# Optimization experiments

Measured on AMD Instinct MI355X. Metric: run time of the kernel, lower is better.

The kernel has to match this reference:

```python
import jax, jax.numpy as jnp
import numpy as np
import math

D_MODEL = 512
N_HEADS = 8
D_FF = 2048
TOP_FACTOR = 5
LN_EPS = 1e-5


def _layernorm(x, g, b):
    m = jnp.mean(x, axis=-1, keepdims=True)
    v = jnp.mean((x - m) ** 2, axis=-1, keepdims=True)
    return (x - m) / jnp.sqrt(v + LN_EPS) * g + b


def _prob_sparse_attn(q_in, k_in, v_in, wq, bq, wk, bk, wv, bv, wo, bo):
    # weights stored (in, out): y = x @ w + b  (equivalent to torch Linear)
    B, Lq, dm = q_in.shape
    Lk = k_in.shape[1]
    H, D = N_HEADS, dm // N_HEADS
    q = (q_in @ wq + bq).reshape(B, Lq, H, D).transpose(0, 2, 1, 3)  # (B,H,Lq,D)
    k = (k_in @ wk + bk).reshape(B, Lk, H, D).transpose(0, 2, 1, 3)
    v = (v_in @ wv + bv).reshape(B, Lk, H, D).transpose(0, 2, 1, 3)

    qn = q / jnp.linalg.norm(q, axis=-1, keepdims=True)
    kn = k / jnp.linalg.norm(k, axis=-1, keepdims=True)
    # full cosine-similarity matrix, reduced to a row mean (as in the original)
    scores_all = jnp.einsum('bhqd,bhkd->bhqk', qn, kn)
    mean_scores = scores_all.mean(axis=-1)  # (B,H,Lq)

    u = max(1, Lq // TOP_FACTOR)
    _, top_idx = jax.lax.top_k(mean_scores, u)  # (B,H,u)

    q_sel = jnp.take_along_axis(q, top_idx[..., None], axis=2)  # (B,H,u,D)
    scores = jnp.einsum('bhud,bhkd->bhuk', q_sel, k) / math.sqrt(D)
    attn = jax.nn.softmax(scores, axis=-1)
    ctx_sel = jnp.einsum('bhuk,bhkd->bhud', attn, v)  # (B,H,u,D)

    b_ix = jnp.arange(B)[:, None, None]
    h_ix = jnp.arange(H)[None, :, None]
    context = jnp.zeros((B, H, Lq, D), dtype=q.dtype).at[b_ix, h_ix, top_idx].set(ctx_sel)
    out = context.transpose(0, 2, 1, 3).reshape(B, Lq, dm)
    return out @ wo + bo


def _decoder_layer(x, enc_out, p):
    xn = _layernorm(x, p['ln1_g'], p['ln1_b'])
    x = x + _prob_sparse_attn(xn, xn, xn, p['sa_wq'], p['sa_bq'], p['sa_wk'], p['sa_bk'],
                              p['sa_wv'], p['sa_bv'], p['sa_wo'], p['sa_bo'])
    xn = _layernorm(x, p['ln2_g'], p['ln2_b'])
    x = x + _prob_sparse_attn(xn, enc_out, enc_out, p['ca_wq'], p['ca_bq'], p['ca_wk'], p['ca_bk'],
                              p['ca_wv'], p['ca_bv'], p['ca_wo'], p['ca_bo'])
    xn = _layernorm(x, p['ln3_g'], p['ln3_b'])
    h = jax.nn.relu(xn @ p['ff_w1'] + p['ff_b1'])
    return x + (h @ p['ff_w2'] + p['ff_b2'])


def setup_inputs() -> dict:
    key = jax.random.key(0)
    ks = iter(jax.random.split(key, 32))
    B, L = 2, 2048
    dm, dff = D_MODEL, D_FF
    s = 1.0 / math.sqrt(dm)
    inp = {
        'x': jax.random.normal(next(ks), (B, L, dm), jnp.float32),
        'enc_out': jax.random.normal(next(ks), (B, L, dm), jnp.float32),
    }
    for pre in ('sa', 'ca'):
        for nm in ('wq', 'wk', 'wv', 'wo'):
            inp[f'{pre}_{nm}'] = jax.random.normal(next(ks), (dm, dm), jnp.float32) * s
            inp[f'{pre}_{nm[1:] and "b" + nm[1:]}'] = jnp.zeros((dm,), jnp.float32)
    inp['ff_w1'] = jax.random.normal(next(ks), (dm, dff), jnp.float32) * s
    inp['ff_b1'] = jnp.zeros((dff,), jnp.float32)
    inp['ff_w2'] = jax.random.normal(next(ks), (dff, dm), jnp.float32) / math.sqrt(dff)
    inp['ff_b2'] = jnp.zeros((dm,), jnp.float32)
    for i in (1, 2, 3):
        inp[f'ln{i}_g'] = jnp.ones((dm,), jnp.float32)
        inp[f'ln{i}_b'] = jnp.zeros((dm,), jnp.float32)
    return inp


def reference(x, enc_out,
              sa_wq, sa_bq, sa_wk, sa_bk, sa_wv, sa_bv, sa_wo, sa_bo,
              ca_wq, ca_bq, ca_wk, ca_bk, ca_wv, ca_bv, ca_wo, ca_bo,
              ff_w1, ff_b1, ff_w2, ff_b2,
              ln1_g, ln1_b, ln2_g, ln2_b, ln3_g, ln3_b):
    p = dict(sa_wq=sa_wq, sa_bq=sa_bq, sa_wk=sa_wk, sa_bk=sa_bk, sa_wv=sa_wv, sa_bv=sa_bv,
             sa_wo=sa_wo, sa_bo=sa_bo, ca_wq=ca_wq, ca_bq=ca_bq, ca_wk=ca_wk, ca_bk=ca_bk,
             ca_wv=ca_wv, ca_bv=ca_bv, ca_wo=ca_wo, ca_bo=ca_bo,
             ff_w1=ff_w1, ff_b1=ff_b1, ff_w2=ff_w2, ff_b2=ff_b2,
             ln1_g=ln1_g, ln1_b=ln1_b, ln2_g=ln2_g, ln2_b=ln2_b, ln3_g=ln3_g, ln3_b=ln3_b)
    return _decoder_layer(x, enc_out, p)
```

## Files before the change

kernel.cpp:

```cpp
#include <hip/hip_runtime.h>

#define BB 2
#define LL 2048
#define DM 512
#define NH 8
#define DH 64
#define DFF 2048
#define UU 409
#define ROWS (BB*LL)
#define X_ELEMS 2097152
#define NCHUNK 8

typedef unsigned short u16;
typedef __attribute__((ext_vector_type(8))) short short8;
typedef __attribute__((ext_vector_type(4))) float floatx4;

#define G_TOTAL 38200000
__device__ float g_buf[G_TOTAL];
__device__ int   g_isbf16;

#define A_Q     10495488
#define A_K     12592640
#define A_V     14689792
#define A_MKN   25175552
#define A_MS    25176576
#define A_RANK  25209344
#define A_PARTK 25242112
#define A_LIST  25274880
#define A_PO    25281536
#define A_PML   29475840
#define A_CTXF  16786944
#define XN_H    16796672
#define XN_L    18893824
#define CTX_H   33573888
#define CTX_L   35671040
#define ENC_H   37768192
#define ENC_L   39865344
#define AH_H    41962496
#define KH16    59213824
#define KL16    61310976
#define VTH16   63408128
#define VTL16   65505280
#define WT_SAQKV 67864576
#define WT_SAO   69437440
#define WT_CAQ   69961728
#define WT_CAKV  70486016
#define WT_CAO   71534592
#define WT_W1    72058880
#define WT_W2    74156032

__constant__ int c_end[28] = {
    2097152, 4194304, 4456448, 4456960, 4719104, 4719616, 4981760, 4982272,
    5244416, 5244928, 5507072, 5507584, 5769728, 5770240, 6032384, 6032896,
    6295040, 6295552, 7344128, 7346176, 8394752, 8395264, 8395776, 8396288,
    8396800, 8397312, 8397824, 8398336
};
__constant__ int sm_idx[16] = {3,5,7,9,11,13,15,17,19,21,22,23,24,25,26,27};
__constant__ int sm_cum[16] = {64,128,192,256,320,384,448,512,768,832,896,960,1024,1088,1152,1216};
#define XG 262144
#define EG 262144
#define SG 1216

__device__ __forceinline__ float bf2f(u16 x) {
    union { unsigned int u; float f; } c; c.u = ((unsigned int)x) << 16; return c.f;
}
__device__ __forceinline__ u16 f2bf(float f) {
    union { float f; unsigned int u; } c; c.f = f;
    unsigned int u = c.u;
    return (u16)((u + 0x7FFFu + ((u >> 16) & 1u)) >> 16);
}

struct P28 { const void* p[28]; };
struct I3 { int v[3]; };

__constant__ int tj[10][6] = {
    {2,  WT_SAQKV, 0,    512,  786432, 8},
    {4,  WT_SAQKV, 512,  512,  786432, 8},
    {6,  WT_SAQKV, 1024, 512,  786432, 8},
    {8,  WT_SAO,   0,    512,  262144, 8},
    {10, WT_CAQ,   0,    512,  262144, 8},
    {12, WT_CAKV,  0,    512,  524288, 8},
    {14, WT_CAKV,  512,  512,  524288, 8},
    {16, WT_CAO,   0,    512,  262144, 8},
    {18, WT_W1,    0,    512, 1048576, 32},
    {20, WT_W2,    0,   2048, 1048576, 8},
};
__constant__ int tcum[10] = {64, 128, 192, 256, 320, 384, 448, 512, 768, 1024};
__global__ void prep_all(P28 ps) {
    const int f = (((const u16*)ps.p[22])[0] == 0x3F80u) ? 1 : 0;
    if (blockIdx.x == 0 && threadIdx.x == 0) g_isbf16 = f;
    u16* gb16 = (u16*)g_buf;
    if (blockIdx.x < 1024) {
        int bid = blockIdx.x;
        int j = 0;
        while (bid >= tcum[j]) j++;
        int t = bid - (j ? tcum[j - 1] : 0);
        int widx = tj[j][0], wt = tj[j][1], col0 = tj[j][2];
        int K = tj[j][3], lo = tj[j][4], txn = tj[j][5];
        int Nsrc = txn * 64;
        int n0 = (t % txn) * 64, k0 = (t / txn) * 64;
        __shared__ float tb[64][65];
        int c = threadIdx.x & 63, r0 = threadIdx.x >> 6;
        const void* W = ps.p[widx];
        u16* WTh = gb16 + wt;
        for (int i = 0; i < 16; i++) {
            int r = r0 + 4 * i;
            size_t src = (size_t)(k0 + r) * Nsrc + n0 + c;
            tb[r][c] = f ? bf2f(((const u16*)W)[src]) : ((const float*)W)[src];
        }
        __syncthreads();
        for (int i = 0; i < 16; i++) {
            int r = r0 + 4 * i;
            float v = tb[c][r];
            u16 hi = f2bf(v);
            size_t o = (size_t)(col0 + n0 + r) * K + k0 + c;
            WTh[o] = hi;
            WTh[lo + o] = f2bf(v - bf2f(hi));
        }
        return;
    }
    int stride = 2048 * blockDim.x;
    for (int g = (blockIdx.x - 1024) * blockDim.x + threadIdx.x; g < XG + EG + SG; g += stride) {
        if (g < XG) {
            int e = g * 8;
            if (f) {
                uint4 raw = ((const uint4*)ps.p[0])[g];
                const u16* rr = (const u16*)&raw;
                float v[8] __attribute__((aligned(16)));
#pragma unroll
                for (int i = 0; i < 8; i++) v[i] = bf2f(rr[i]);
                *(float4*)(g_buf + e) = ((const float4*)v)[0];
                *(float4*)(g_buf + e + 4) = ((const float4*)v)[1];
            } else {
                *(uint4*)(g_buf + e)     = ((const uint4*)ps.p[0])[g * 2];
                *(uint4*)(g_buf + e + 4) = ((const uint4*)ps.p[0])[g * 2 + 1];
            }
        } else if (g < XG + EG) {
            int gl = g - XG;
            int e = gl * 8;
            float v[8] __attribute__((aligned(16)));
            if (f) {
                uint4 raw = ((const uint4*)ps.p[1])[gl];
                const u16* rr = (const u16*)&raw;
#pragma unroll
                for (int i = 0; i < 8; i++) v[i] = bf2f(rr[i]);
            } else {
                *(float4*)(v)     = ((const float4*)ps.p[1])[gl * 2];
                *(float4*)(v + 4) = ((const float4*)ps.p[1])[gl * 2 + 1];
            }
            u16 hh[8] __attribute__((aligned(16)));
            u16 lo[8] __attribute__((aligned(16)));
#pragma unroll
            for (int i = 0; i < 8; i++) { u16 hi = f2bf(v[i]); hh[i] = hi; lo[i] = f2bf(v[i] - bf2f(hi)); }
            *(uint4*)(&gb16[ENC_H + e]) = *(const uint4*)hh;
            *(uint4*)(&gb16[ENC_L + e]) = *(const uint4*)lo;
        } else {
            int t = g - XG - EG;
            int si = 0;
            while (t >= sm_cum[si]) si++;
            int s = sm_idx[si];
            int gl = t - (si ? sm_cum[si - 1] : 0);
            int e = gl * 8;
            float* dst = g_buf + c_end[s - 1] + e;
            if (f) {
                uint4 raw = *(const uint4*)((const u16*)ps.p[s] + e);
                const u16* rr = (const u16*)&raw;
#pragma unroll
                for (int i = 0; i < 8; i++) dst[i] = bf2f(rr[i]);
            } else {
                *(uint4*)(dst)     = *(const uint4*)((const float*)ps.p[s] + e);
                *(uint4*)(dst + 4) = *(const uint4*)((const float*)ps.p[s] + e + 4);
            }
        }
    }
}

__global__ void lnorm_k(int x_off, int g_off, int b_off, int yh_u16, int yl_u16) {
    int row = blockIdx.x;
    int tid = threadIdx.x;
    const float* x = g_buf + x_off + (size_t)row * DM;
    float a = x[tid], c = x[tid + 256];
    float s1 = a + c, s2 = a * a + c * c;
    for (int o = 32; o > 0; o >>= 1) { s1 += __shfl_xor(s1, o); s2 += __shfl_xor(s2, o); }
    __shared__ float r1[4], r2[4];
    int wave = tid >> 6, lane = tid & 63;
    if (lane == 0) { r1[wave] = s1; r2[wave] = s2; }
    __syncthreads();
    s1 = r1[0] + r1[1] + r1[2] + r1[3];
    s2 = r2[0] + r2[1] + r2[2] + r2[3];
    float mean = s1 * (1.0f / DM);
    float var  = s2 * (1.0f / DM) - mean * mean;
    float rstd = rsqrtf(var + 1e-5f);
    const float* gg = g_buf + g_off;
    const float* bb = g_buf + b_off;
    u16* yh = ((u16*)g_buf) + yh_u16 + (size_t)row * DM;
    u16* yl = ((u16*)g_buf) + yl_u16 + (size_t)row * DM;
    float v1 = (a - mean) * rstd * gg[tid]       + bb[tid];
    float v2 = (c - mean) * rstd * gg[tid + 256] + bb[tid + 256];
    u16 h1 = f2bf(v1), h2 = f2bf(v2);
    yh[tid] = h1;       yl[tid] = f2bf(v1 - bf2f(h1));
    yh[tid + 256] = h2; yl[tid + 256] = f2bf(v2 - bf2f(h2));
}

template<int WM, bool SPLIT, bool SEC, bool RELU, bool RESID, bool FINAL, bool OUTH>
__global__ void mgemm_k(I3 a_offs, I3 splt, I3 alz, int wt_u16_off, I3 boffs, int resid_off,
                        int out_off, void* __restrict__ dext, int M, int N, int K) {
    constexpr int BT_M = WM * 32;
    constexpr int A4 = BT_M * 4;
    __shared__ u16 Ash[BT_M * 40];
    __shared__ u16 Asl[SPLIT ? BT_M * 40 : 8];
    __shared__ u16 Bsh[128 * 40];
    __shared__ u16 Bsl[SPLIT ? 128 * 40 : 8];
    int sec_blk = SEC ? ((blockIdx.x * 128) >> 9) : 0;
    const u16* Ah = ((const u16*)g_buf) + a_offs.v[sec_blk];
    const u16* Al = Ah + (size_t)M * K;
    const u16* WTh = ((const u16*)g_buf) + wt_u16_off;
    const u16* WTl = WTh + (size_t)N * K;
    const int isbf = g_isbf16;
    const bool use_al = SPLIT && splt.v[sec_blk] && !(alz.v[sec_blk] && isbf);
    const bool use_bl = SPLIT && splt.v[sec_blk] && !isbf;
    int tid = threadIdx.x;
    int lane = tid & 63, wid = tid >> 6;
    int wm = wid >> 1, wn = wid & 1;
    int quad = lane >> 4, l15 = lane & 15;
    int m0 = blockIdx.y * BT_M, n0 = blockIdx.x * 128;
    floatx4 acc[WM][4];
#pragma unroll
    for (int i = 0; i < WM; i++)
#pragma unroll
        for (int j = 0; j < 4; j++) acc[i][j] = (floatx4){0.f, 0.f, 0.f, 0.f};
    for (int k0 = 0; k0 < K; k0 += 32) {
#pragma unroll
        for (int i = 0; i < (A4 + 255) / 256; i++) {
            int idx8 = tid + 256 * i;
            if (A4 % 256 == 0 || idx8 < A4) {
                int r = idx8 >> 2, c8 = (idx8 & 3) * 8;
                *(uint4*)(&Ash[r * 40 + c8]) = *(const uint4*)(Ah + (size_t)(m0 + r) * K + k0 + c8);
                if (SPLIT && use_al)
                    *(uint4*)(&Asl[r * 40 + c8]) = *(const uint4*)(Al + (size_t)(m0 + r) * K + k0 + c8);
            }
        }
#pragma unroll
        for (int i = 0; i < 2; i++) {
            int idx8 = tid + 256 * i;
            int r = idx8 >> 2, c8 = (idx8 & 3) * 8;
            *(uint4*)(&Bsh[r * 40 + c8]) = *(const uint4*)(WTh + (size_t)(n0 + r) * K + k0 + c8);
            if (SPLIT && use_bl)
                *(uint4*)(&Bsl[r * 40 + c8]) = *(const uint4*)(WTl + (size_t)(n0 + r) * K + k0 + c8);
        }
        __syncthreads();
        short8 ah[WM], bh[4], al[WM], bl[4];
#pragma unroll
        for (int i = 0; i < WM; i++) {
            int ro = (wm * WM * 16 + i * 16 + l15) * 40 + quad * 8;
            ah[i] = *(const short8*)(&Ash[ro]);
            if (SPLIT && use_al) al[i] = *(const short8*)(&Asl[ro]);
        }
#pragma unroll
        for (int j = 0; j < 4; j++) {
            int ro = (wn * 64 + j * 16 + l15) * 40 + quad * 8;
            bh[j] = *(const short8*)(&Bsh[ro]);
            if (SPLIT && use_bl) bl[j] = *(const short8*)(&Bsl[ro]);
        }
#pragma unroll
        for (int i = 0; i < WM; i++)
#pragma unroll
            for (int j = 0; j < 4; j++) {
                acc[i][j] = __builtin_amdgcn_mfma_f32_16x16x32_bf16(ah[i], bh[j], acc[i][j], 0, 0, 0);
                if constexpr (SPLIT) {
                    if (use_bl)
                        acc[i][j] = __builtin_amdgcn_mfma_f32_16x16x32_bf16(ah[i], bl[j], acc[i][j], 0, 0, 0);
                    if (use_al)
                        acc[i][j] = __builtin_amdgcn_mfma_f32_16x16x32_bf16(al[i], bh[j], acc[i][j], 0, 0, 0);
                }
            }
        __syncthreads();
    }
#pragma unroll
    for (int i = 0; i < WM; i++)
#pragma unroll
        for (int j = 0; j < 4; j++)
#pragma unroll
            for (int r = 0; r < 4; r++) {
                int row = m0 + wm * WM * 16 + i * 16 + quad * 4 + r;
                int col = n0 + wn * 64 + j * 16 + l15;
                int sec = SEC ? (col >> 9) : 0;
                int ci  = SEC ? (col & 511) : col;
                float v = acc[i][j][r] + g_buf[boffs.v[sec] + ci];
                if (RELU) v = fmaxf(v, 0.f);
                if (RESID) v += g_buf[resid_off + (size_t)row * N + col];
                if (FINAL) {
                    if (g_isbf16) ((u16*)dext)[(size_t)row * N + col] = f2bf(v);
                    else          ((float*)dext)[(size_t)row * N + col] = v;
                } else if (OUTH) {
                    ((u16*)g_buf)[out_off + (size_t)row * N + col] = f2bf(v);
                } else if (SEC) {
                    g_buf[out_off + ((size_t)sec * ROWS + row) * 512 + ci] = v;
                } else {
                    g_buf[out_off + (size_t)row * N + col] = v;
                }
            }
}

__global__ void meankn_p1(int k_off, int part_off) {
    int bh = blockIdx.x >> 5, chunk = blockIdx.x & 31;
    int b = bh >> 3, h = bh & 7;
    int wave = threadIdx.x >> 6, lane = threadIdx.x & 63;
    const float* base = g_buf + k_off + (size_t)b * LL * DM + (size_t)h * DH + lane;
    float acc = 0.f;
    for (int t = 0; t < 16; t++) {
        int j = chunk * 64 + wave * 16 + t;
        float kv = base[(size_t)j * DM];
        float s = kv * kv;
        for (int o = 32; o > 0; o >>= 1) s += __shfl_xor(s, o);
        acc += kv / sqrtf(fmaxf(s, 1e-30f));
    }
    __shared__ float red[4][64];
    red[wave][lane] = acc;
    __syncthreads();
    if (threadIdx.x < 64)
        g_buf[part_off + (size_t)blockIdx.x * 64 + threadIdx.x] =
            red[0][threadIdx.x] + red[1][threadIdx.x] + red[2][threadIdx.x] + red[3][threadIdx.x];
}

__global__ void mscore_k(int q_off, int part_off, int ms_off) {
    int bh = blockIdx.y, b = bh >> 3, h = bh & 7;
    int tid = threadIdx.x;
    __shared__ float mk[64];
    if (tid < 64) {
        float s = 0.f;
        for (int c = 0; c < 32; c++) s += g_buf[part_off + (size_t)(bh * 32 + c) * 64 + tid];
        mk[tid] = s * (1.0f / LL);
    }
    __syncthreads();
    int w = tid >> 6, lane = tid & 63;
    float m = mk[lane];
#pragma unroll
    for (int it = 0; it < 8; it++) {
        int row = blockIdx.x * 32 + it * 4 + w;
        float qv = g_buf[q_off + ((size_t)b * LL + row) * DM + h * DH + lane];
        float s = qv * qv, d = qv * m;
        for (int o = 32; o > 0; o >>= 1) { s += __shfl_xor(s, o); d += __shfl_xor(d, o); }
        if (lane == 0) g_buf[ms_off + bh * LL + row] = d / sqrtf(fmaxf(s, 1e-30f));
    }
}

__global__ void topsel_k(int ms_off, int list_off, int rank_off, int u) {
    __shared__ float s[LL];
    int bh = blockIdx.y, chunk = blockIdx.x;
    for (int i = threadIdx.x; i < LL; i += 256) s[i] = g_buf[ms_off + bh * LL + i];
    __syncthreads();
    int il = threadIdx.x >> 2;
    int i = chunk * 64 + il;
    int jq = threadIdx.x & 3;
    float si = s[i];
    int cnt = 0;
    for (int t = 0; t < 512; t++) {
        int j = jq * 512 + t;
        float sj = s[j];
        cnt += (sj > si) || (sj == si && j < i);
    }
    cnt += __shfl_xor(cnt, 1);
    cnt += __shfl_xor(cnt, 2);
    if (jq == 0) {
        int* list = (int*)(g_buf + list_off);
        int* rank = (int*)(g_buf + rank_off);
        if (cnt < u) { list[bh * 416 + cnt] = i; rank[bh * LL + i] = cnt; }
        else rank[bh * LL + i] = -1;
    }
}

template<bool LO>
__global__ void kvprep_k(int k_off, int v_off) {
    int bh = blockIdx.y, b = bh >> 3, h = bh & 7;
    int tok0 = blockIdx.x * 64;
    int tid = threadIdx.x;
    __shared__ float vt[64][68];
    u16* gb16 = (u16*)g_buf;
    int tok = tid >> 2, dq = (tid & 3) * 16;
    const float* kp = g_buf + k_off + ((size_t)(b * LL + tok0 + tok)) * DM + h * DH + dq;
    const float* vp = g_buf + v_off + ((size_t)(b * LL + tok0 + tok)) * DM + h * DH + dq;
    float kv[16] __attribute__((aligned(16)));
#pragma unroll
    for (int i = 0; i < 4; i++) *(float4*)(kv + 4 * i) = *(const float4*)(kp + 4 * i);
    u16 hh[16] __attribute__((aligned(16)));
    u16 lo[16] __attribute__((aligned(16)));
#pragma unroll
    for (int i = 0; i < 16; i++) { hh[i] = f2bf(kv[i]); if (LO) lo[i] = f2bf(kv[i] - bf2f(hh[i])); }
    size_t ko = ((size_t)(bh * LL + tok0 + tok)) * DH + dq;
    *(uint4*)(gb16 + KH16 + ko)     = ((const uint4*)hh)[0];
    *(uint4*)(gb16 + KH16 + ko + 8) = ((const uint4*)hh)[1];
    if (LO) {
        *(uint4*)(gb16 + KL16 + ko)     = ((const uint4*)lo)[0];
        *(uint4*)(gb16 + KL16 + ko + 8) = ((const uint4*)lo)[1];
    }
#pragma unroll
    for (int i = 0; i < 4; i++) *(float4*)(&vt[tok][dq + 4 * i]) = *(const float4*)(vp + 4 * i);
    __syncthreads();
    int d = tid >> 2, tq = (tid & 3) * 16;
    float vv[16];
#pragma unroll
    for (int i = 0; i < 16; i++) vv[i] = vt[tq + i][d];
#pragma unroll
    for (int i = 0; i < 16; i++) { hh[i] = f2bf(vv[i]); if (LO) lo[i] = f2bf(vv[i] - bf2f(hh[i])); }
    size_t vo = ((size_t)(bh * DH + d)) * LL + tok0 + tq;
    *(uint4*)(gb16 + VTH16 + vo)     = ((const uint4*)hh)[0];
    *(uint4*)(gb16 + VTH16 + vo + 8) = ((const uint4*)hh)[1];
    if (LO) {
        *(uint4*)(gb16 + VTL16 + vo)     = ((const uint4*)lo)[0];
        *(uint4*)(gb16 + VTL16 + vo + 8) = ((const uint4*)lo)[1];
    }
}

template<bool S3>
__global__ __launch_bounds__(256, 4) void attn_flash(int q_off, int kh_off, int kl_off,
        int vth_off, int vtl_off, int list_off, int po_off, int pml_off, int u) {
    int bid = blockIdx.x;
    int grp = bid & 127;
    int sxt = bid >> 7;
    int bh = grp & 15, chunk = grp >> 4;
    int b = bh >> 3, h = bh & 7;
    int tid = threadIdx.x, lane = tid & 63, w = tid >> 6;
    int quad = lane >> 4, l15 = lane & 15;
    const int* list = (const int*)(g_buf + list_off);

    short8 qh[2], ql[2];
    {
        int slot_q = sxt * 64 + w * 16 + l15;
        int qidx = list[bh * 416 + (slot_q < u ? slot_q : u - 1)];
        const float* qp = g_buf + q_off + ((size_t)b * LL + qidx) * DM + h * DH;
#pragma unroll
        for (int d2 = 0; d2 < 2; d2++) {
            float v[8] __attribute__((aligned(16)));
            *(float4*)(v)     = *(const float4*)(qp + d2 * 32 + quad * 8);
            *(float4*)(v + 4) = *(const float4*)(qp + d2 * 32 + quad * 8 + 4);
            u16 hh[8] __attribute__((aligned(16)));
            u16 lo[8] __attribute__((aligned(16)));
#pragma unroll
            for (int j = 0; j < 8; j++) {
                float s = v[j] * 0.125f;
                u16 hi = f2bf(s); hh[j] = hi; lo[j] = f2bf(s - bf2f(hi));
            }
            qh[d2] = *(const short8*)hh; ql[d2] = *(const short8*)lo;
        }
    }

    __shared__ u16 Ksh[32 * 68];
    __shared__ u16 Ksl[S3 ? 32 * 68 : 8];
    __shared__ u16 Vth[64 * 36];
    __shared__ u16 Vtl[S3 ? 64 * 36 : 8];
    __shared__ float ps_all[4][16 * 36];

    const u16* gb16 = (const u16*)g_buf;
    const u16* KHp = gb16 + kh_off + (size_t)bh * LL * DH;
    const u16* KLp = gb16 + kl_off + (size_t)bh * LL * DH;
    const u16* VHp = gb16 + vth_off + (size_t)bh * DH * LL;
    const u16* VLp = gb16 + vtl_off + (size_t)bh * DH * LL;
    int krow = tid >> 3, kcol = (tid & 7) * 8;
    int vd = tid >> 2, vcol = (tid & 3) * 8;

    uint4 pre[S3 ? 4 : 2];
    auto issue = [&](int row0) {
        pre[0] = *(const uint4*)(KHp + (size_t)(row0 + krow) * DH + kcol);
        pre[1] = *(const uint4*)(VHp + (size_t)vd * LL + row0 + vcol);
        if constexpr (S3) {
            pre[2] = *(const uint4*)(KLp + (size_t)(row0 + krow) * DH + kcol);
            pre[3] = *(const uint4*)(VLp + (size_t)vd * LL + row0 + vcol);
        }
    };
    auto commit = [&]() {
        *(uint4*)(&Ksh[krow * 68 + kcol]) = pre[0];
        *(uint4*)(&Vth[vd * 36 + vcol]) = pre[1];
        if constexpr (S3) {
            *(uint4*)(&Ksl[krow * 68 + kcol]) = pre[2];
            *(uint4*)(&Vtl[vd * 36 + vcol]) = pre[3];
        }
    };

    float m_run[4], l_run[4];
    floatx4 acc_o[4];
#pragma unroll
    for (int r = 0; r < 4; r++) {
        m_run[r] = -3.0e38f; l_run[r] = 0.f;
        acc_o[r] = (floatx4){0.f, 0.f, 0.f, 0.f};
    }

    issue(chunk * 256);
    for (int kt = 0; kt < 8; ++kt) {
        __syncthreads();
        commit();
        if (kt < 7) issue(chunk * 256 + (kt + 1) * 32);
        __syncthreads();
        float* ps = ps_all[w];
        floatx4 sacc[2];
#pragma unroll
        for (int t = 0; t < 2; t++) {
            sacc[t] = (floatx4){0.f, 0.f, 0.f, 0.f};
#pragma unroll
            for (int d2 = 0; d2 < 2; d2++) {
                int ro = (t * 16 + l15) * 68 + d2 * 32 + quad * 8;
                short8 kh = *(const short8*)(&Ksh[ro]);
                sacc[t] = __builtin_amdgcn_mfma_f32_16x16x32_bf16(qh[d2], kh, sacc[t], 0, 0, 0);
                sacc[t] = __builtin_amdgcn_mfma_f32_16x16x32_bf16(ql[d2], kh, sacc[t], 0, 0, 0);
                if constexpr (S3) {
                    short8 kl = *(const short8*)(&Ksl[ro]);
                    sacc[t] = __builtin_amdgcn_mfma_f32_16x16x32_bf16(qh[d2], kl, sacc[t], 0, 0, 0);
                }
            }
        }
        float alpha[4];
#pragma unroll
        for (int r = 0; r < 4; r++) {
            float mx = fmaxf(sacc[0][r], sacc[1][r]);
            for (int o = 1; o < 16; o <<= 1) mx = fmaxf(mx, __shfl_xor(mx, o));
            float mn = fmaxf(m_run[r], mx);
            alpha[r] = __expf(m_run[r] - mn);
            m_run[r] = mn;
            float p0 = __expf(sacc[0][r] - mn);
            float p1 = __expf(sacc[1][r] - mn);
            sacc[0][r] = p0; sacc[1][r] = p1;
            float ls = p0 + p1;
            for (int o = 1; o < 16; o <<= 1) ls += __shfl_xor(ls, o);
            l_run[r] = l_run[r] * alpha[r] + ls;
        }
#pragma unroll
        for (int t = 0; t < 2; t++)
#pragma unroll
            for (int r = 0; r < 4; r++)
                ps[(quad * 4 + r) * 36 + t * 16 + l15] = sacc[t][r];
#pragma unroll
        for (int j = 0; j < 4; j++)
#pragma unroll
            for (int r = 0; r < 4; r++) acc_o[j][r] *= alpha[r];
        float pv[8] __attribute__((aligned(16)));
        *(float4*)(pv)     = *(const float4*)(&ps[l15 * 36 + quad * 8]);
        *(float4*)(pv + 4) = *(const float4*)(&ps[l15 * 36 + quad * 8 + 4]);
        u16 ph[8] __attribute__((aligned(16)));
        u16 pl[8] __attribute__((aligned(16)));
#pragma unroll
        for (int j = 0; j < 8; j++) { u16 hi = f2bf(pv[j]); ph[j] = hi; pl[j] = f2bf(pv[j] - bf2f(hi)); }
        short8 phv = *(const short8*)ph, plv = *(const short8*)pl;
#pragma unroll
        for (int j = 0; j < 4; j++) {
            int ro = (j * 16 + l15) * 36 + quad * 8;
            short8 vh = *(const short8*)(&Vth[ro]);
            acc_o[j] = __builtin_amdgcn_mfma_f32_16x16x32_bf16(phv, vh, acc_o[j], 0, 0, 0);
            acc_o[j] = __builtin_amdgcn_mfma_f32_16x16x32_bf16(plv, vh, acc_o[j], 0, 0, 0);
            if constexpr (S3) {
                short8 vl = *(const short8*)(&Vtl[ro]);
                acc_o[j] = __builtin_amdgcn_mfma_f32_16x16x32_bf16(phv, vl, acc_o[j], 0, 0, 0);
            }
        }
    }
#pragma unroll
    for (int r = 0; r < 4; r++) {
        int slot = sxt * 64 + w * 16 + quad * 4 + r;
        if (slot >= u) continue;
        size_t rec = ((size_t)(bh * NCHUNK + chunk)) * 512 + slot;
        float* po = g_buf + po_off + rec * 64;
#pragma unroll
        for (int j = 0; j < 4; j++) po[j * 16 + l15] = acc_o[j][r];
        if (l15 == 0) {
            float* pml = g_buf + pml_off + rec * 2;
            pml[0] = m_run[r]; pml[1] = l_run[r];
        }
    }
}

__global__ void attn_combine(int po_off, int pml_off, int rank_off, int u) {
    int bh = blockIdx.y;
    int b = bh >> 3, h = bh & 7;
    int tid = threadIdx.x;
    int qi = tid >> 4;
    int kb = tid & 15;
    int ds = kb * 4;
    int row = blockIdx.x * 16 + qi;
    int rank = ((const int*)(g_buf + rank_off))[bh * LL + row];
    size_t idx = ((size_t)b * LL + row) * DM + h * DH + ds;
    if (rank < 0) {
        ushort4 z = {0, 0, 0, 0};
        *(ushort4*)(((u16*)g_buf) + CTX_H + idx) = z;
        *(ushort4*)(((u16*)g_buf) + CTX_L + idx) = z;
        return;
    }
    float m = -3.0e38f;
#pragma unroll
    for (int c = 0; c < NCHUNK; c++)
        m = fmaxf(m, g_buf[pml_off + (((size_t)(bh * NCHUNK + c)) * 512 + rank) * 2]);
    float l = 0.f, O0 = 0.f, O1 = 0.f, O2 = 0.f, O3 = 0.f;
#pragma unroll
    for (int c = 0; c < NCHUNK; c++) {
        size_t rec = ((size_t)(bh * NCHUNK + c)) * 512 + rank;
        const float* pml = g_buf + pml_off + rec * 2;
        float a = __expf(pml[0] - m);
        l += a * pml[1];
        float4 o = *(const float4*)(g_buf + po_off + rec * 64 + ds);
        O0 += a * o.x; O1 += a * o.y; O2 += a * o.z; O3 += a * o.w;
    }
    float inv = 1.0f / l;
    float o0 = O0 * inv, o1 = O1 * inv, o2 = O2 * inv, o3 = O3 * inv;
    ushort4 hv, lv;
    hv.x = f2bf(o0); lv.x = f2bf(o0 - bf2f(hv.x));
    hv.y = f2bf(o1); lv.y = f2bf(o1 - bf2f(hv.y));
    hv.z = f2bf(o2); lv.z = f2bf(o2 - bf2f(hv.z));
    hv.w = f2bf(o3); lv.w = f2bf(o3 - bf2f(hv.w));
    *(ushort4*)(((u16*)g_buf) + CTX_H + idx) = hv;
    *(ushort4*)(((u16*)g_buf) + CTX_L + idx) = lv;
}

extern "C" void kernel_launch(void* const* d_in, const int* in_sizes, int n_in,
                              void* d_out, int out_size, void* d_ws, size_t ws_size,
                              hipStream_t stream) {
    static const int SZ[28] = {
        2097152, 2097152,
        262144, 512, 262144, 512, 262144, 512, 262144, 512,
        262144, 512, 262144, 512, 262144, 512, 262144, 512,
        1048576, 2048, 1048576, 512,
        512, 512, 512, 512, 512, 512
    };
    int OFF[28];
    int cur = 0;
    for (int i = 0; i < 28; i++) { OFF[i] = cur; cur += SZ[i]; }

    P28 ps;
    for (int i = 0; i < 28; i++) ps.p[i] = d_in[i];
    prep_all<<<3072, 256, 0, stream>>>(ps);

    auto select_attend = [&](bool sa) {
        if (sa) kvprep_k<true><<<dim3(32, 16), 256, 0, stream>>>(A_K, A_V);
        else    kvprep_k<false><<<dim3(32, 16), 256, 0, stream>>>(A_K, A_V);
        meankn_p1<<<16 * 32, 256, 0, stream>>>(A_K, A_PARTK);
        mscore_k<<<dim3(64, 16), 256, 0, stream>>>(A_Q, A_PARTK, A_MS);
        topsel_k<<<dim3(32, 16), 256, 0, stream>>>(A_MS, A_LIST, A_RANK, UU);
        if (sa)
            attn_flash<true><<<896, 256, 0, stream>>>(
                A_Q, KH16, KL16, VTH16, VTL16, A_LIST, A_PO, A_PML, UU);
        else
            attn_flash<false><<<896, 256, 0, stream>>>(
                A_Q, KH16, KL16, VTH16, VTL16, A_LIST, A_PO, A_PML, UU);
        attn_combine<<<dim3(128, 16), 256, 0, stream>>>(A_PO, A_PML, A_RANK, UU);
    };

    lnorm_k<<<ROWS, 256, 0, stream>>>(OFF[0], OFF[22], OFF[23], XN_H, XN_L);
    mgemm_k<2, true, true, false, false, false, false><<<dim3(12, 64), 256, 0, stream>>>(
        I3{{XN_H, XN_H, XN_H}}, I3{{1, 1, 1}}, I3{{0, 0, 0}},
        WT_SAQKV, I3{{OFF[3], OFF[5], OFF[7]}}, 0, A_Q, nullptr, ROWS, 1536, 512);
    select_attend(true);
    mgemm_k<1, true, false, false, true, false, false><<<dim3(4, 128), 256, 0, stream>>>(
        I3{{CTX_H, 0, 0}}, I3{{1, 0, 0}}, I3{{0, 0, 0}},
        WT_SAO, I3{{OFF[9], 0, 0}}, OFF[0], OFF[0], nullptr, ROWS, 512, 512);

    lnorm_k<<<ROWS, 256, 0, stream>>>(OFF[0], OFF[24], OFF[25], XN_H, XN_L);
    mgemm_k<1, true, false, false, false, false, false><<<dim3(4, 128), 256, 0, stream>>>(
        I3{{XN_H, 0, 0}}, I3{{1, 0, 0}}, I3{{0, 0, 0}},
        WT_CAQ, I3{{OFF[11], 0, 0}}, 0, A_Q, nullptr, ROWS, 512, 512);
    mgemm_k<2, true, true, false, false, false, false><<<dim3(8, 64), 256, 0, stream>>>(
        I3{{ENC_H, ENC_H, ENC_H}}, I3{{1, 0, 0}}, I3{{1, 0, 0}},
        WT_CAKV, I3{{OFF[13], OFF[15], 0}}, 0, A_K, nullptr, ROWS, 1024, 512);
    select_attend(false);
    mgemm_k<1, false, false, false, true, false, false><<<dim3(4, 128), 256, 0, stream>>>(
        I3{{CTX_H, 0, 0}}, I3{{0, 0, 0}}, I3{{0, 0, 0}},
        WT_CAO, I3{{OFF[17], 0, 0}}, OFF[0], OFF[0], nullptr, ROWS, 512, 512);

    lnorm_k<<<ROWS, 256, 0, stream>>>(OFF[0], OFF[26], OFF[27], XN_H, XN_L);
    mgemm_k<4, false, false, true, false, false, true><<<dim3(16, 32), 256, 0, stream>>>(
        I3{{XN_H, 0, 0}}, I3{{0, 0, 0}}, I3{{0, 0, 0}},
        WT_W1, I3{{OFF[19], 0, 0}}, 0, AH_H, nullptr, ROWS, 2048, 512);
    mgemm_k<1, false, false, false, true, true, false><<<dim3(4, 128), 256, 0, stream>>>(
        I3{{AH_H, 0, 0}}, I3{{0, 0, 0}}, I3{{0, 0, 0}},
        WT_W2, I3{{OFF[21], 0, 0}}, OFF[0], 0, d_out, ROWS, 512, 2048);
}
```

Measured before the change: 576.1 us.

## Transpose attention MFMAs to keep P in registers via bpermute instead of LDS

The QK and PV MFMA operands are swapped so each lane owns one query row. The softmax max and sum reductions then shrink to two cross-lane shuffles, and m/l become scalars per lane. The P tile is split into hi/lo parts with packed bf16 conversion instructions and redistributed across lanes with ds_bpermute, replacing the shared-memory staging buffer. Outputs are written as float4 per row. This removes the LDS round trip and scalar conversions but adds many bpermute operations and selects.

```diff
diff --git a/kernel.cpp b/kernel.cpp
--- a/kernel.cpp
+++ b/kernel.cpp
@@ -68,6 +68,11 @@
     union { float f; unsigned int u; } c; c.f = f;
     unsigned int u = c.u;
     return (u16)((u + 0x7FFFu + ((u >> 16) & 1u)) >> 16);
+}
+__device__ __forceinline__ unsigned cvtpk_bf16(float a, float b) {
+    unsigned r;
+    asm("v_cvt_pk_bf16_f32 %0, %1, %2" : "=v"(r) : "v"(a), "v"(b));
+    return r;
 }
 
 struct P28 { const void* p[28]; };
@@ -449,7 +454,6 @@
     __shared__ u16 Ksl[S3 ? 32 * 68 : 8];
     __shared__ u16 Vth[64 * 36];
     __shared__ u16 Vtl[S3 ? 64 * 36 : 8];
-    __shared__ float ps_all[4][16 * 36];
 
     const u16* gb16 = (const u16*)g_buf;
     const u16* KHp = gb16 + kh_off + (size_t)bh * LL * DH;
@@ -459,6 +463,10 @@
     int krow = tid >> 3, kcol = (tid & 7) * 8;
     int vd = tid >> 2, vcol = (tid & 3) * 8;
 
+    int aA = ((((lane >> 4) & 1) << 5) | l15) << 2;
+    int aB = aA + 64;
+    bool hiT = (quad >= 2);
+
     uint4 pre[S3 ? 4 : 2];
     auto issue = [&](int row0) {
         pre[0] = *(const uint4*)(KHp + (size_t)(row0 + krow) * DH + kcol);
@@ -477,13 +485,10 @@
         }
     };
 
-    float m_run[4], l_run[4];
+    float m_run = -3.0e38f, l_run = 0.f;
     floatx4 acc_o[4];
 #pragma unroll
-    for (int r = 0; r < 4; r++) {
-        m_run[r] = -3.0e38f; l_run[r] = 0.f;
-        acc_o[r] = (floatx4){0.f, 0.f, 0.f, 0.f};
-    }
+    for (int j = 0; j < 4; j++) acc_o[j] = (floatx4){0.f, 0.f, 0.f, 0.f};
 
     issue(chunk * 256);
     for (int kt = 0; kt < 8; ++kt) {
@@ -491,7 +496,6 @@
         commit();
         if (kt < 7) issue(chunk * 256 + (kt + 1) * 32);
         __syncthreads();
-        float* ps = ps_all[w];
         floatx4 sacc[2];
 #pragma unroll
         for (int t = 0; t < 2; t++) {
@@ -500,69 +504,84 @@
             for (int d2 = 0; d2 < 2; d2++) {
                 int ro = (t * 16 + l15) * 68 + d2 * 32 + quad * 8;
                 short8 kh = *(const short8*)(&Ksh[ro]);
-                sacc[t] = __builtin_amdgcn_mfma_f32_16x16x32_bf16(qh[d2], kh, sacc[t], 0, 0, 0);
-                sacc[t] = __builtin_amdgcn_mfma_f32_16x16x32_bf16(ql[d2], kh, sacc[t], 0, 0, 0);
+                sacc[t] = __builtin_amdgcn_mfma_f32_16x16x32_bf16(kh, qh[d2], sacc[t], 0, 0, 0);
+                sacc[t] = __builtin_amdgcn_mfma_f32_16x16x32_bf16(kh, ql[d2], sacc[t], 0, 0, 0);
                 if constexpr (S3) {
                     short8 kl = *(const short8*)(&Ksl[ro]);
-                    sacc[t] = __builtin_amdgcn_mfma_f32_16x16x32_bf16(qh[d2], kl, sacc[t], 0, 0, 0);
+                    sacc[t] = __builtin_amdgcn_mfma_f32_16x16x32_bf16(kl, qh[d2], sacc[t], 0, 0, 0);
                 }
             }
         }
-        float alpha[4];
-#pragma unroll
-        for (int r = 0; r < 4; r++) {
-            float mx = fmaxf(sacc[0][r], sacc[1][r]);
-            for (int o = 1; o < 16; o <<= 1) mx = fmaxf(mx, __shfl_xor(mx, o));
-            float mn = fmaxf(m_run[r], mx);
-            alpha[r] = __expf(m_run[r] - mn);
-            m_run[r] = mn;
-            float p0 = __expf(sacc[0][r] - mn);
-            float p1 = __expf(sacc[1][r] - mn);
-            sacc[0][r] = p0; sacc[1][r] = p1;
-            float ls = p0 + p1;
-            for (int o = 1; o < 16; o <<= 1) ls += __shfl_xor(ls, o);
-            l_run[r] = l_run[r] * alpha[r] + ls;
-        }
+        float mx = fmaxf(fmaxf(fmaxf(sacc[0][0], sacc[0][1]), fmaxf(sacc[0][2], sacc[0][3])),
+                         fmaxf(fmaxf(sacc[1][0], sacc[1][1]), fmaxf(sacc[1][2], sacc[1][3])));
+        mx = fmaxf(mx, __shfl_xor(mx, 16));
+        mx = fmaxf(mx, __shfl_xor(mx, 32));
+        float mn = fmaxf(m_run, mx);
+        float alpha = __expf(m_run - mn);
+        m_run = mn;
 #pragma unroll
         for (int t = 0; t < 2; t++)
 #pragma unroll
-            for (int r = 0; r < 4; r++)
-                ps[(quad * 4 + r) * 36 + t * 16 + l15] = sacc[t][r];
+            for (int r = 0; r < 4; r++) sacc[t][r] = __expf(sacc[t][r] - mn);
+        float ls = (sacc[0][0] + sacc[0][1]) + (sacc[0][2] + sacc[0][3])
+                 + (sacc[1][0] + sacc[1][1]) + (sacc[1][2] + sacc[1][3]);
+        ls += __shfl_xor(ls, 16);
+        ls += __shfl_xor(ls, 32);
+        l_run = l_run * alpha + ls;
+        unsigned phw[2][2], plw[2][2];
+#pragma unroll
+        for (int t = 0; t < 2; t++)
+#pragma unroll
+            for (int hh = 0; hh < 2; hh++) {
+                float s0 = sacc[t][2 * hh], s1 = sacc[t][2 * hh + 1];
+                unsigned hw = cvtpk_bf16(s0, s1);
+                phw[t][hh] = hw;
+                float r0 = s0 - __uint_as_float(hw << 16);
+                float r1 = s1 - __uint_as_float(hw & 0xFFFF0000u);
+                plw[t][hh] = cvtpk_bf16(r0, r1);
+            }
+        union { unsigned wd[4]; short8 v; } pbh, pbl;
+#pragma unroll
+        for (int hh = 0; hh < 2; hh++) {
+            int a0 = __builtin_amdgcn_ds_bpermute(aA, (int)phw[0][hh]);
+            int a1 = __builtin_amdgcn_ds_bpermute(aA, (int)phw[1][hh]);
+            pbh.wd[hh] = (unsigned)(hiT ? a1 : a0);
+            int b0 = __builtin_amdgcn_ds_bpermute(aB, (int)phw[0][hh]);
+            int b1 = __builtin_amdgcn_ds_bpermute(aB, (int)phw[1][hh]);
+            pbh.wd[2 + hh] = (unsigned)(hiT ? b1 : b0);
+            int c0 = __builtin_amdgcn_ds_bpermute(aA, (int)plw[0][hh]);
+            int c1 = __builtin_amdgcn_ds_bpermute(aA, (int)plw[1][hh]);
+            pbl.wd[hh] = (unsigned)(hiT ? c1 : c0);
+            int d0 = __builtin_amdgcn_ds_bpermute(aB, (int)plw[0][hh]);
+            int d1 = __builtin_amdgcn_ds_bpermute(aB, (int)plw[1][hh]);
+            pbl.wd[2 + hh] = (unsigned)(hiT ? d1 : d0);
+        }
 #pragma unroll
         for (int j = 0; j < 4; j++)
 #pragma unroll
-            for (int r = 0; r < 4; r++) acc_o[j][r] *= alpha[r];
-        float pv[8] __attribute__((aligned(16)));
-        *(float4*)(pv)     = *(const float4*)(&ps[l15 * 36 + quad * 8]);
-        *(float4*)(pv + 4) = *(const float4*)(&ps[l15 * 36 + quad * 8 + 4]);
-        u16 ph[8] __attribute__((aligned(16)));
-        u16 pl[8] __attribute__((aligned(16)));
-#pragma unroll
-        for (int j = 0; j < 8; j++) { u16 hi = f2bf(pv[j]); ph[j] = hi; pl[j] = f2bf(pv[j] - bf2f(hi)); }
-        short8 phv = *(const short8*)ph, plv = *(const short8*)pl;
+            for (int r = 0; r < 4; r++) acc_o[j][r] *= alpha;
 #pragma unroll
         for (int j = 0; j < 4; j++) {
             int ro = (j * 16 + l15) * 36 + quad * 8;
             short8 vh = *(const short8*)(&Vth[ro]);
-            acc_o[j] = __builtin_amdgcn_mfma_f32_16x16x32_bf16(phv, vh, acc_o[j], 0, 0, 0);
-            acc_o[j] = __builtin_amdgcn_mfma_f32_16x16x32_bf16(plv, vh, acc_o[j], 0, 0, 0);
+            acc_o[j] = __builtin_amdgcn_mfma_f32_16x16x32_bf16(vh, pbh.v, acc_o[j], 0, 0, 0);
+            acc_o[j] = __builtin_amdgcn_mfma_f32_16x16x32_bf16(vh, pbl.v, acc_o[j], 0, 0, 0);
             if constexpr (S3) {
                 short8 vl = *(const short8*)(&Vtl[ro]);
-                acc_o[j] = __builtin_amdgcn_mfma_f32_16x16x32_bf16(phv, vl, acc_o[j], 0, 0, 0);
-            }
-        }
-    }
-#pragma unroll
-    for (int r = 0; r < 4; r++) {
-        int slot = sxt * 64 + w * 16 + quad * 4 + r;
-        if (slot >= u) continue;
+                acc_o[j] = __builtin_amdgcn_mfma_f32_16x16x32_bf16(vl, pbh.v, acc_o[j], 0, 0, 0);
+            }
+        }
+    }
+    int slot = sxt * 64 + w * 16 + l15;
+    if (slot < u) {
         size_t rec = ((size_t)(bh * NCHUNK + chunk)) * 512 + slot;
         float* po = g_buf + po_off + rec * 64;
 #pragma unroll
-        for (int j = 0; j < 4; j++) po[j * 16 + l15] = acc_o[j][r];
-        if (l15 == 0) {
+        for (int j = 0; j < 4; j++)
+            *(float4*)(po + j * 16 + quad * 4) = *(const float4*)&acc_o[j];
+        if (quad == 0) {
             float* pml = g_buf + pml_off + rec * 2;
-            pml[0] = m_run[r]; pml[1] = l_run[r];
+            pml[0] = m_run; pml[1] = l_run;
         }
     }
 }
```

Result: no change. 578.6 us (+0.4%).
